# Kernel tuning notes

Measured on AMD Instinct MI355X. Metric: run time of the kernel, lower is better.

The kernel has to match this reference:

```python
import jax, jax.numpy as jnp
import numpy as np

H = 4       # N_head
C = 32      # c_hidden
CZ = 128    # c_z
N = 256
B = 1
EPS = 1e-5


def setup_inputs() -> dict:
    key = jax.random.key(0)
    ks = jax.random.split(key, 8)
    hc = H * C
    return {
        "z": jax.random.normal(ks[0], (B, N, N, CZ), dtype=jnp.float32),
        "ln_scale": jnp.ones((CZ,), dtype=jnp.float32),
        "ln_bias": jnp.zeros((CZ,), dtype=jnp.float32),
        "Wq": jax.random.normal(ks[1], (CZ, hc), dtype=jnp.float32) * 0.02,
        "Wk": jax.random.normal(ks[2], (CZ, hc), dtype=jnp.float32) * 0.02,
        "Wv": jax.random.normal(ks[3], (CZ, hc), dtype=jnp.float32) * 0.02,
        "Wb": jax.random.normal(ks[4], (CZ, H), dtype=jnp.float32) * 0.02,
        "Wg": jax.random.normal(ks[5], (CZ, hc), dtype=jnp.float32) * 0.02,
        "Wo": jax.random.normal(ks[6], (hc, CZ), dtype=jnp.float32) * 0.02,
    }


def reference(z, ln_scale, ln_bias, Wq, Wk, Wv, Wb, Wg, Wo):
    b, n = z.shape[0], z.shape[1]
    # LayerNorm over c_z
    mu = jnp.mean(z, axis=-1, keepdims=True)
    var = jnp.mean(jnp.square(z - mu), axis=-1, keepdims=True)
    zn = (z - mu) * jax.lax.rsqrt(var + EPS) * ln_scale + ln_bias
    # projections -> [B, N, N, H, C]
    q = (zn @ Wq).reshape(b, n, n, H, C)
    k = (zn @ Wk).reshape(b, n, n, H, C)
    v = (zn @ Wv).reshape(b, n, n, H, C)
    bias = zn @ Wb                                  # [B, N, N, H]
    g = jax.nn.sigmoid(zn @ Wg).reshape(b, n, n, H, C)
    # attention around starting node i: query at (i,j), keys/values at (i,k)
    scores = jnp.einsum('bijhd,bikhd->bijkh', q, k) * (1.0 / C ** 0.5)
    scores = scores + bias[:, None, :, :, :]        # bias[b, j, k, h]
    a = jax.nn.softmax(scores, axis=-2)             # softmax over k
    o = jnp.einsum('bijkh,bikhd->bijhd', a, v)      # [B, N, N, H, C]
    o = (g * o).reshape(b, n, n, H * C)
    return o @ Wo
```

## Files before the change

kernel.cpp:

```cpp
#include <hip/hip_runtime.h>
#include <math.h>

#define NN 256
#define CZ 128
#define NH 4
#define CH 32
#define HC 128
#define NPIX (NN*NN)
#define L2E   1.4426950408889634f
#define SCALE2 (0.17677669529663687f * 1.4426950408889634f)

typedef __attribute__((ext_vector_type(8))) short bf16x8;
typedef __attribute__((ext_vector_type(4))) float fx4;
typedef __attribute__((ext_vector_type(4))) unsigned u32x4;

__device__ __forceinline__ unsigned pack_hl(float x) {
    unsigned b  = __builtin_bit_cast(unsigned, x);
    unsigned hb = b & 0xFFFF0000u;
    float r = x - __builtin_bit_cast(float, hb);
    return hb | (__builtin_bit_cast(unsigned, r) >> 16);
}
__device__ __forceinline__ void load_split8(const float* p, bf16x8& h, bf16x8& l) {
    float4 x0 = *(const float4*)p;
    float4 x1 = *(const float4*)(p + 4);
    float xs[8] = {x0.x, x0.y, x0.z, x0.w, x1.x, x1.y, x1.z, x1.w};
    #pragma unroll
    for (int j = 0; j < 8; ++j) {
        unsigned b  = __builtin_bit_cast(unsigned, xs[j]);
        unsigned hb = b & 0xFFFF0000u;
        float r = xs[j] - __builtin_bit_cast(float, hb);
        h[j] = (short)(hb >> 16);
        l[j] = (short)(__builtin_bit_cast(unsigned, r) >> 16);
    }
}
__device__ __forceinline__ void deint_raw(u32x4 e0, u32x4 e1, bf16x8& h, bf16x8& l) {
    unsigned es[8] = {e0[0], e0[1], e0[2], e0[3], e1[0], e1[1], e1[2], e1[3]};
    unsigned hw[4], lw[4];
    #pragma unroll
    for (int j = 0; j < 4; ++j) {
        unsigned a = es[2 * j], b = es[2 * j + 1];
        hw[j] = (a >> 16) | (b & 0xFFFF0000u);
        lw[j] = (a & 0x0000FFFFu) | (b << 16);
    }
    h = __builtin_bit_cast(bf16x8, u32x4{hw[0], hw[1], hw[2], hw[3]});
    l = __builtin_bit_cast(bf16x8, u32x4{lw[0], lw[1], lw[2], lw[3]});
}
__device__ __forceinline__ void deint8(const unsigned* p, bf16x8& h, bf16x8& l) {
    u32x4 e0 = *(const u32x4*)p;
    u32x4 e1 = *(const u32x4*)(p + 4);
    deint_raw(e0, e1, h, l);
}

__device__ __forceinline__ void qtrans(unsigned &x, unsigned &y) {
#if __has_builtin(__builtin_amdgcn_permlane32_swap) && __has_builtin(__builtin_amdgcn_permlane16_swap)
    {
        auto r = __builtin_amdgcn_permlane32_swap(x, y, false, false);
        x = r[0]; y = r[1];
    }
    {
        auto r = __builtin_amdgcn_permlane16_swap(x, y, false, false);
        x = r[0]; y = r[1];
    }
#else
    asm("v_permlane32_swap_b32 %0, %1\n\t"
        "v_permlane16_swap_b32 %0, %1" : "+v"(x), "+v"(y));
#endif
}

__global__ __launch_bounds__(256) void pack_w_kernel(
    const float* __restrict__ Wq, const float* __restrict__ Wk,
    const float* __restrict__ Wv, const float* __restrict__ Wg,
    const float* __restrict__ Wo, bf16x8* __restrict__ pk)
{
    int id  = blockIdx.x * 256 + threadIdx.x;
    int mid = id >> 11;
    int e   = id & 2047;
    const float* W = (mid == 0) ? Wq : (mid == 1) ? Wk : (mid == 2) ? Wv : (mid == 3) ? Wg : Wo;
    int quad = e & 3, n = (e >> 2) & 127, ks = e >> 9;
    int k0 = ks * 32 + quad * 8;
    bf16x8 h, l;
    #pragma unroll
    for (int j = 0; j < 8; ++j) {
        float x = W[(size_t)(k0 + j) * 128 + n];
        unsigned b  = __builtin_bit_cast(unsigned, x);
        unsigned hb = b & 0xFFFF0000u;
        float r = x - __builtin_bit_cast(float, hb);
        h[j] = (short)(hb >> 16);
        l[j] = (short)(__builtin_bit_cast(unsigned, r) >> 16);
    }
    pk[(size_t)mid * 4096 + e]        = h;
    pk[(size_t)mid * 4096 + 2048 + e] = l;
}

__global__ __launch_bounds__(256) void ln_proj_kernel(
    const float* __restrict__ z, const float* __restrict__ ls, const float* __restrict__ lb,
    const float* __restrict__ Wb, const bf16x8* __restrict__ pk,
    unsigned* __restrict__ q_pk, unsigned* __restrict__ k_pk, unsigned* __restrict__ v_pk,
    float* __restrict__ g_ws, float* __restrict__ bias_n)
{
    __shared__ float zsh[32][132];
    __shared__ float rsum[256], rsq[256];
    __shared__ float pmu[32], prs[32];

    const int t  = threadIdx.x;
    const int p0 = blockIdx.x * 32;
    const int i  = p0 >> 8;
    const int j0 = p0 & 255;

    const float4* z4 = (const float4*)(z + (size_t)p0 * CZ);
    #pragma unroll
    for (int r = 0; r < 4; ++r) {
        int idx4 = t + 256 * r;
        int p = idx4 >> 5, pos = idx4 & 31;
        *(float4*)&zsh[p][pos * 4] = z4[idx4];
    }
    __syncthreads();

    {
        int p = t >> 3, sg = t & 7;
        float s = 0.f, q = 0.f;
        #pragma unroll
        for (int u = 0; u < 16; ++u) { float x = zsh[p][sg * 16 + u]; s += x; q += x * x; }
        rsum[t] = s; rsq[t] = q;
    }
    __syncthreads();
    if (t < 32) {
        float s = 0.f, q = 0.f;
        #pragma unroll
        for (int g = 0; g < 8; ++g) { s += rsum[t * 8 + g]; q += rsq[t * 8 + g]; }
        float mu  = s * (1.0f / 128.0f);
        float var = q * (1.0f / 128.0f) - mu * mu;
        float a   = var + 1e-5f;
        float r   = rsqrtf(a);
        r = r * (1.5f - 0.5f * a * r * r);
        pmu[t] = mu; prs[t] = r;
    }
    __syncthreads();

    #pragma unroll
    for (int r4 = 0; r4 < 4; ++r4) {
        int idx4 = t + 256 * r4;
        int p = idx4 >> 5, pos = idx4 & 31;
        float4 v  = *(float4*)&zsh[p][pos * 4];
        float4 s4 = ((const float4*)ls)[pos];
        float4 b4 = ((const float4*)lb)[pos];
        float mu = pmu[p], rs = prs[p];
        v.x = (v.x - mu) * rs * s4.x + b4.x;
        v.y = (v.y - mu) * rs * s4.y + b4.y;
        v.z = (v.z - mu) * rs * s4.z + b4.z;
        v.w = (v.w - mu) * rs * s4.w + b4.w;
        *(float4*)&zsh[p][pos * 4] = v;
    }
    __syncthreads();

    const int wv = t >> 6, lane = t & 63;
    const int lrow = lane & 15, quad = lane >> 4;
    const bf16x8* ph = pk + (size_t)wv * 4096;
    const bf16x8* pl = ph + 2048;

    fx4 acc[2][8];
    #pragma unroll
    for (int mr = 0; mr < 2; ++mr)
        #pragma unroll
        for (int nc = 0; nc < 8; ++nc)
            acc[mr][nc] = fx4{0.f, 0.f, 0.f, 0.f};

    #pragma unroll
    for (int ks = 0; ks < 4; ++ks) {
        bf16x8 ah[2], al[2];
        #pragma unroll
        for (int mr = 0; mr < 2; ++mr)
            load_split8(&zsh[mr * 16 + lrow][ks * 32 + quad * 8], ah[mr], al[mr]);
        #pragma unroll
        for (int nc = 0; nc < 8; ++nc) {
            int bi = (ks * 128 + nc * 16 + lrow) * 4 + quad;
            bf16x8 bh = ph[bi], bl = pl[bi];
            #pragma unroll
            for (int mr = 0; mr < 2; ++mr) {
                acc[mr][nc] = __builtin_amdgcn_mfma_f32_16x16x32_bf16(ah[mr], bl, acc[mr][nc], 0, 0, 0);
                acc[mr][nc] = __builtin_amdgcn_mfma_f32_16x16x32_bf16(al[mr], bh, acc[mr][nc], 0, 0, 0);
                acc[mr][nc] = __builtin_amdgcn_mfma_f32_16x16x32_bf16(ah[mr], bh, acc[mr][nc], 0, 0, 0);
            }
        }
    }

    #pragma unroll
    for (int mr = 0; mr < 2; ++mr) {
        #pragma unroll
        for (int nc = 0; nc < 8; ++nc) {
            int cg = nc * 16 + lrow;
            int h = cg >> 5, cc = cg & 31;
            int jl = mr * 16 + quad * 4;
            fx4 a = acc[mr][nc];
            if (wv == 0) {
                unsigned* qp = q_pk + ((size_t)(i * NH + h) * NN + j0 + jl) * CH + cc;
                #pragma unroll
                for (int r = 0; r < 4; ++r) qp[r * CH] = pack_hl(a[r]);
            } else if (wv == 1) {
                unsigned* kp = k_pk + ((size_t)(i * NH + h) * NN + j0 + jl) * CH + cc;
                #pragma unroll
                for (int r = 0; r < 4; ++r) kp[r * CH] = pack_hl(a[r]);
            } else if (wv == 2) {
                u32x4 e = {pack_hl(a[0]), pack_hl(a[1]), pack_hl(a[2]), pack_hl(a[3])};
                *(u32x4*)(v_pk + ((size_t)(i * NH + h) * CH + cc) * NN + j0 + jl) = e;
            } else {
                float* gp = g_ws + (size_t)(p0 + jl) * HC + cg;
                #pragma unroll
                for (int r = 0; r < 4; ++r) gp[r * HC] = 1.0f / (1.0f + __expf(-a[r]));
            }
        }
    }

    if (t < 128) {
        int hh = t >> 5, p = t & 31;
        float b = 0.f;
        for (int d = 0; d < 128; ++d) b = fmaf(zsh[p][d], Wb[d * 4 + hh], b);
        bias_n[(size_t)hh * NPIX + (size_t)i * NN + j0 + p] = b * L2E;
    }
}

__global__ __launch_bounds__(256) void attn_kernel(
    const unsigned* __restrict__ q_pk, const unsigned* __restrict__ k_pk,
    const unsigned* __restrict__ v_pk, const float* __restrict__ g_ws,
    const float* __restrict__ bias_n, float* __restrict__ go_ws)
{
    const int t = threadIdx.x;
    const int wv = t >> 6, lane = t & 63;
    const int lrow = lane & 15, quad = lane >> 4;
    const int h = blockIdx.x & 3, i = blockIdx.x >> 2;
    const int qb = wv * 64;

    const unsigned* qs = q_pk + (size_t)(i * NH + h) * NN * CH;
    const unsigned* ks = k_pk + (size_t)(i * NH + h) * NN * CH;
    const unsigned* vs = v_pk + (size_t)(i * NH + h) * CH * NN;
    const float*    bs = bias_n + (size_t)h * NPIX;

    bf16x8 qh[4], ql[4];
    #pragma unroll
    for (int nt = 0; nt < 4; ++nt)
        deint8(qs + (size_t)(qb + nt * 16 + lrow) * CH + quad * 8, qh[nt], ql[nt]);

    u32x4 krA[2], krB[2];
    #pragma unroll
    for (int mt = 0; mt < 2; ++mt) {
        const u32x4* kp = (const u32x4*)(ks + (size_t)(mt * 16 + lrow) * CH + quad * 8);
        krA[mt] = kp[0]; krB[mt] = kp[1];
    }

    fx4 oacc[2][4];
    #pragma unroll
    for (int ct = 0; ct < 2; ++ct)
        #pragma unroll
        for (int nt = 0; nt < 4; ++nt)
            oacc[ct][nt] = fx4{0.f, 0.f, 0.f, 0.f};
    float lsum[4] = {0.f, 0.f, 0.f, 0.f};

    for (int kb = 0; kb < NN; kb += 32) {
        u32x4 vrA[2], vrB[2];
        #pragma unroll
        for (int ct = 0; ct < 2; ++ct) {
            const u32x4* vp = (const u32x4*)(vs + (size_t)(ct * 16 + lrow) * NN + kb + quad * 8);
            vrA[ct] = vp[0]; vrB[ct] = vp[1];
        }
        float4 bv[4][2];
        #pragma unroll
        for (int nt = 0; nt < 4; ++nt)
            #pragma unroll
            for (int mt = 0; mt < 2; ++mt)
                bv[nt][mt] = *(const float4*)(bs + (size_t)(qb + nt * 16 + lrow) * NN
                                                 + kb + mt * 16 + quad * 4);
        const int kb2 = (kb + 32) & (NN - 1);
        u32x4 nkA[2], nkB[2];
        #pragma unroll
        for (int mt = 0; mt < 2; ++mt) {
            const u32x4* kp = (const u32x4*)(ks + (size_t)(kb2 + mt * 16 + lrow) * CH + quad * 8);
            nkA[mt] = kp[0]; nkB[mt] = kp[1];
        }

        bf16x8 kh[2], kl_[2];
        #pragma unroll
        for (int mt = 0; mt < 2; ++mt)
            deint_raw(krA[mt], krB[mt], kh[mt], kl_[mt]);

        fx4 sv[4][2];
        __builtin_amdgcn_s_setprio(1);
        #pragma unroll
        for (int nt = 0; nt < 4; ++nt) {
            #pragma unroll
            for (int mt = 0; mt < 2; ++mt) {
                fx4 s = fx4{0.f, 0.f, 0.f, 0.f};
                s = __builtin_amdgcn_mfma_f32_16x16x32_bf16(kh[mt],  ql[nt], s, 0, 0, 0);
                s = __builtin_amdgcn_mfma_f32_16x16x32_bf16(kl_[mt], qh[nt], s, 0, 0, 0);
                s = __builtin_amdgcn_mfma_f32_16x16x32_bf16(kh[mt],  qh[nt], s, 0, 0, 0);
                sv[nt][mt] = s;
            }
        }
        __builtin_amdgcn_s_setprio(0);

        bf16x8 vh[2], vl[2];
        #pragma unroll
        for (int ct = 0; ct < 2; ++ct)
            deint_raw(vrA[ct], vrB[ct], vh[ct], vl[ct]);

        unsigned w0h[4][2], w1h[4][2], w0l[4][2], w1l[4][2];
        #pragma unroll
        for (int nt = 0; nt < 4; ++nt) {
            #pragma unroll
            for (int mt = 0; mt < 2; ++mt) {
                fx4 s = sv[nt][mt];
                float4 b4 = bv[nt][mt];
                float e0 = exp2f(fmaf(s[0], SCALE2, b4.x));
                float e1 = exp2f(fmaf(s[1], SCALE2, b4.y));
                float e2 = exp2f(fmaf(s[2], SCALE2, b4.z));
                float e3 = exp2f(fmaf(s[3], SCALE2, b4.w));
                lsum[nt] += (e0 + e1) + (e2 + e3);

                unsigned b0 = __builtin_bit_cast(unsigned, e0);
                unsigned b1 = __builtin_bit_cast(unsigned, e1);
                unsigned b2 = __builtin_bit_cast(unsigned, e2);
                unsigned b3 = __builtin_bit_cast(unsigned, e3);
                unsigned h01 = (b0 >> 16) | (b1 & 0xFFFF0000u);
                unsigned h23 = (b2 >> 16) | (b3 & 0xFFFF0000u);
                float r0 = e0 - __builtin_bit_cast(float, b0 & 0xFFFF0000u);
                float r1 = e1 - __builtin_bit_cast(float, b1 & 0xFFFF0000u);
                float r2 = e2 - __builtin_bit_cast(float, b2 & 0xFFFF0000u);
                float r3 = e3 - __builtin_bit_cast(float, b3 & 0xFFFF0000u);
                unsigned l01 = (__builtin_bit_cast(unsigned, r0) >> 16)
                             | (__builtin_bit_cast(unsigned, r1) & 0xFFFF0000u);
                unsigned l23 = (__builtin_bit_cast(unsigned, r2) >> 16)
                             | (__builtin_bit_cast(unsigned, r3) & 0xFFFF0000u);
                w0h[nt][mt] = h01; w1h[nt][mt] = h23;
                w0l[nt][mt] = l01; w1l[nt][mt] = l23;
            }
        }

        #pragma unroll
        for (int nt = 0; nt < 4; ++nt) {
            qtrans(w0h[nt][0], w0h[nt][1]);
            qtrans(w1h[nt][0], w1h[nt][1]);
            qtrans(w0l[nt][0], w0l[nt][1]);
            qtrans(w1l[nt][0], w1l[nt][1]);
        }

        __builtin_amdgcn_s_setprio(1);
        #pragma unroll
        for (int nt = 0; nt < 4; ++nt) {
            bf16x8 pbh = __builtin_bit_cast(bf16x8,
                u32x4{w0h[nt][0], w1h[nt][0], w0h[nt][1], w1h[nt][1]});
            bf16x8 pbl = __builtin_bit_cast(bf16x8,
                u32x4{w0l[nt][0], w1l[nt][0], w0l[nt][1], w1l[nt][1]});
            #pragma unroll
            for (int ct = 0; ct < 2; ++ct) {
                oacc[ct][nt] = __builtin_amdgcn_mfma_f32_16x16x32_bf16(vh[ct], pbl, oacc[ct][nt], 0, 0, 0);
                oacc[ct][nt] = __builtin_amdgcn_mfma_f32_16x16x32_bf16(vl[ct], pbh, oacc[ct][nt], 0, 0, 0);
                oacc[ct][nt] = __builtin_amdgcn_mfma_f32_16x16x32_bf16(vh[ct], pbh, oacc[ct][nt], 0, 0, 0);
            }
        }
        __builtin_amdgcn_s_setprio(0);

        #pragma unroll
        for (int mt = 0; mt < 2; ++mt) { krA[mt] = nkA[mt]; krB[mt] = nkB[mt]; }
    }

    #pragma unroll
    for (int nt = 0; nt < 4; ++nt) {
        float s = lsum[nt];
        s += __shfl_xor(s, 16, 64);
        s += __shfl_xor(s, 32, 64);
        float inv = 1.0f / s;
        size_t pix = (size_t)i * NN + qb + nt * 16 + lrow;
        #pragma unroll
        for (int ct = 0; ct < 2; ++ct) {
            const float* gp = g_ws + pix * HC + h * CH + ct * 16 + quad * 4;
            float4 g4 = *(const float4*)gp;
            fx4 o = oacc[ct][nt];
            float4 r;
            r.x = g4.x * o[0] * inv;
            r.y = g4.y * o[1] * inv;
            r.z = g4.z * o[2] * inv;
            r.w = g4.w * o[3] * inv;
            *(float4*)(go_ws + pix * HC + h * CH + ct * 16 + quad * 4) = r;
        }
    }
}

__global__ __launch_bounds__(256) void outproj_kernel(
    const float* __restrict__ go_ws, const bf16x8* __restrict__ pk, float* __restrict__ out)
{
    __shared__ float gsh[64][132];
    const int t  = threadIdx.x;
    const int p0 = blockIdx.x * 64;

    const float4* g4 = (const float4*)(go_ws + (size_t)p0 * HC);
    #pragma unroll
    for (int r = 0; r < 8; ++r) {
        int idx4 = t + 256 * r;
        int p = idx4 >> 5, pos = idx4 & 31;
        *(float4*)&gsh[p][pos * 4] = g4[idx4];
    }
    __syncthreads();

    const int wv = t >> 6, lane = t & 63;
    const int lrow = lane & 15, quad = lane >> 4;
    const bf16x8* ph = pk + (size_t)4 * 4096;
    const bf16x8* pl = ph + 2048;

    fx4 acc[8];
    #pragma unroll
    for (int nc = 0; nc < 8; ++nc) acc[nc] = fx4{0.f, 0.f, 0.f, 0.f};

    #pragma unroll
    for (int ks = 0; ks < 4; ++ks) {
        bf16x8 ah, al;
        load_split8(&gsh[wv * 16 + lrow][ks * 32 + quad * 8], ah, al);
        #pragma unroll
        for (int nc = 0; nc < 8; ++nc) {
            int bi = (ks * 128 + nc * 16 + lrow) * 4 + quad;
            bf16x8 bh = ph[bi], bl = pl[bi];
            acc[nc] = __builtin_amdgcn_mfma_f32_16x16x32_bf16(ah, bl, acc[nc], 0, 0, 0);
            acc[nc] = __builtin_amdgcn_mfma_f32_16x16x32_bf16(al, bh, acc[nc], 0, 0, 0);
            acc[nc] = __builtin_amdgcn_mfma_f32_16x16x32_bf16(ah, bh, acc[nc], 0, 0, 0);
        }
    }

    #pragma unroll
    for (int nc = 0; nc < 8; ++nc) {
        #pragma unroll
        for (int r = 0; r < 4; ++r)
            out[(size_t)(p0 + wv * 16 + quad * 4 + r) * HC + nc * 16 + lrow] = acc[nc][r];
    }
}

extern "C" void kernel_launch(void* const* d_in, const int* in_sizes, int n_in,
                              void* d_out, int out_size, void* d_ws, size_t ws_size,
                              hipStream_t stream)
{
    const float* z  = (const float*)d_in[0];
    const float* ls = (const float*)d_in[1];
    const float* lb = (const float*)d_in[2];
    const float* Wq = (const float*)d_in[3];
    const float* Wk = (const float*)d_in[4];
    const float* Wv = (const float*)d_in[5];
    const float* Wb = (const float*)d_in[6];
    const float* Wg = (const float*)d_in[7];
    const float* Wo = (const float*)d_in[8];

    float* ws = (float*)d_ws;
    const size_t BIG = (size_t)NPIX * HC;
    unsigned* q_pk  = (unsigned*)ws;
    unsigned* k_pk  = (unsigned*)(ws + BIG);
    unsigned* v_pk  = (unsigned*)(ws + 2 * BIG);
    float* g_ws     = ws + 3 * BIG;
    float* go_ws    = ws + 4 * BIG;
    float* bias_n   = ws + 5 * BIG;
    bf16x8* pk      = (bf16x8*)(bias_n + (size_t)NH * NPIX);

    pack_w_kernel<<<40, 256, 0, stream>>>(Wq, Wk, Wv, Wg, Wo, pk);
    ln_proj_kernel<<<NPIX / 32, 256, 0, stream>>>(z, ls, lb, Wb, pk,
                                                  q_pk, k_pk, v_pk, g_ws, bias_n);
    attn_kernel<<<NN * NH, 256, 0, stream>>>(q_pk, k_pk, v_pk, g_ws, bias_n, go_ws);
    outproj_kernel<<<NPIX / 64, 256, 0, stream>>>(go_ws, pk, (float*)d_out);
}
```

Measured before the change: 246.5 us.

## Use register LayerNorm with shuffles, stage Wb in LDS, and skip LDS in outproj

The LayerNorm step now loads each pixel's row directly into registers and reduces the sum and sum of squares with warp shuffles. This replaces the LDS partial-sum arrays and two of the block barriers. The bias projection now reads Wb from shared memory and uses all 256 threads, with pairs of threads splitting the reduction dimension. The output projection loads the gated activations straight from global memory into registers instead of staging them through LDS, which removes a barrier but makes the global reads less coalesced.

Measured after the change: 246.2 us. Within noise of the previous version (-0.2%).

```diff
diff --git a/kernel.cpp b/kernel.cpp
--- a/kernel.cpp
+++ b/kernel.cpp
@@ -99,57 +99,52 @@
     float* __restrict__ g_ws, float* __restrict__ bias_n)
 {
     __shared__ float zsh[32][132];
-    __shared__ float rsum[256], rsq[256];
-    __shared__ float pmu[32], prs[32];
+    __shared__ float wbsh[512];
 
     const int t  = threadIdx.x;
     const int p0 = blockIdx.x * 32;
     const int i  = p0 >> 8;
     const int j0 = p0 & 255;
 
-    const float4* z4 = (const float4*)(z + (size_t)p0 * CZ);
+    wbsh[t]       = Wb[t];
+    wbsh[t + 256] = Wb[t + 256];
+
+    const int p = t >> 3, sub = t & 7;
+    float4 zv[4];
+    {
+        const float4* zp = (const float4*)(z + (size_t)(p0 + p) * CZ + sub * 16);
+        #pragma unroll
+        for (int r = 0; r < 4; ++r) zv[r] = zp[r];
+    }
+    float s = 0.f, q = 0.f;
     #pragma unroll
     for (int r = 0; r < 4; ++r) {
-        int idx4 = t + 256 * r;
-        int p = idx4 >> 5, pos = idx4 & 31;
-        *(float4*)&zsh[p][pos * 4] = z4[idx4];
-    }
-    __syncthreads();
-
+        s += ((zv[r].x + zv[r].y) + (zv[r].z + zv[r].w));
+        q += ((zv[r].x * zv[r].x + zv[r].y * zv[r].y)
+            + (zv[r].z * zv[r].z + zv[r].w * zv[r].w));
+    }
+    #pragma unroll
+    for (int m = 1; m <= 4; m <<= 1) {
+        s += __shfl_xor(s, m, 64);
+        q += __shfl_xor(q, m, 64);
+    }
     {
-        int p = t >> 3, sg = t & 7;
-        float s = 0.f, q = 0.f;
-        #pragma unroll
-        for (int u = 0; u < 16; ++u) { float x = zsh[p][sg * 16 + u]; s += x; q += x * x; }
-        rsum[t] = s; rsq[t] = q;
-    }
-    __syncthreads();
-    if (t < 32) {
-        float s = 0.f, q = 0.f;
-        #pragma unroll
-        for (int g = 0; g < 8; ++g) { s += rsum[t * 8 + g]; q += rsq[t * 8 + g]; }
         float mu  = s * (1.0f / 128.0f);
         float var = q * (1.0f / 128.0f) - mu * mu;
         float a   = var + 1e-5f;
-        float r   = rsqrtf(a);
-        r = r * (1.5f - 0.5f * a * r * r);
-        pmu[t] = mu; prs[t] = r;
-    }
-    __syncthreads();
-
-    #pragma unroll
-    for (int r4 = 0; r4 < 4; ++r4) {
-        int idx4 = t + 256 * r4;
-        int p = idx4 >> 5, pos = idx4 & 31;
-        float4 v  = *(float4*)&zsh[p][pos * 4];
-        float4 s4 = ((const float4*)ls)[pos];
-        float4 b4 = ((const float4*)lb)[pos];
-        float mu = pmu[p], rs = prs[p];
-        v.x = (v.x - mu) * rs * s4.x + b4.x;
-        v.y = (v.y - mu) * rs * s4.y + b4.y;
-        v.z = (v.z - mu) * rs * s4.z + b4.z;
-        v.w = (v.w - mu) * rs * s4.w + b4.w;
-        *(float4*)&zsh[p][pos * 4] = v;
+        float r0  = rsqrtf(a);
+        r0 = r0 * (1.5f - 0.5f * a * r0 * r0);
+        #pragma unroll
+        for (int r = 0; r < 4; ++r) {
+            float4 s4 = ((const float4*)ls)[sub * 4 + r];
+            float4 b4 = ((const float4*)lb)[sub * 4 + r];
+            float4 v  = zv[r];
+            v.x = (v.x - mu) * r0 * s4.x + b4.x;
+            v.y = (v.y - mu) * r0 * s4.y + b4.y;
+            v.z = (v.z - mu) * r0 * s4.z + b4.z;
+            v.w = (v.w - mu) * r0 * s4.w + b4.w;
+            *(float4*)&zsh[p][sub * 16 + r * 4] = v;
+        }
     }
     __syncthreads();
 
@@ -211,11 +206,17 @@
         }
     }
 
-    if (t < 128) {
-        int hh = t >> 5, p = t & 31;
+    {
+        int pair = t >> 1, half = t & 1;
+        int hh = pair >> 5, pp = pair & 31;
+        int d0 = half * 64;
         float b = 0.f;
-        for (int d = 0; d < 128; ++d) b = fmaf(zsh[p][d], Wb[d * 4 + hh], b);
-        bias_n[(size_t)hh * NPIX + (size_t)i * NN + j0 + p] = b * L2E;
+        #pragma unroll 8
+        for (int d = 0; d < 64; ++d)
+            b = fmaf(zsh[pp][d0 + d], wbsh[(d0 + d) * 4 + hh], b);
+        b += __shfl_xor(b, 1, 64);
+        if (half == 0)
+            bias_n[(size_t)hh * NPIX + (size_t)i * NN + j0 + pp] = b * L2E;
     }
 }
 
@@ -387,39 +388,33 @@
 __global__ __launch_bounds__(256) void outproj_kernel(
     const float* __restrict__ go_ws, const bf16x8* __restrict__ pk, float* __restrict__ out)
 {
-    __shared__ float gsh[64][132];
     const int t  = threadIdx.x;
     const int p0 = blockIdx.x * 64;
-
-    const float4* g4 = (const float4*)(go_ws + (size_t)p0 * HC);
-    #pragma unroll
-    for (int r = 0; r < 8; ++r) {
-        int idx4 = t + 256 * r;
-        int p = idx4 >> 5, pos = idx4 & 31;
-        *(float4*)&gsh[p][pos * 4] = g4[idx4];
-    }
-    __syncthreads();
-
     const int wv = t >> 6, lane = t & 63;
     const int lrow = lane & 15, quad = lane >> 4;
     const bf16x8* ph = pk + (size_t)4 * 4096;
     const bf16x8* pl = ph + 2048;
 
+    const float* grow = go_ws + (size_t)(p0 + wv * 16 + lrow) * HC + quad * 8;
+
+    bf16x8 ah[4], al[4];
+    #pragma unroll
+    for (int ks = 0; ks < 4; ++ks)
+        load_split8(grow + ks * 32, ah[ks], al[ks]);
+
     fx4 acc[8];
     #pragma unroll
     for (int nc = 0; nc < 8; ++nc) acc[nc] = fx4{0.f, 0.f, 0.f, 0.f};
 
     #pragma unroll
     for (int ks = 0; ks < 4; ++ks) {
-        bf16x8 ah, al;
-        load_split8(&gsh[wv * 16 + lrow][ks * 32 + quad * 8], ah, al);
         #pragma unroll
         for (int nc = 0; nc < 8; ++nc) {
             int bi = (ks * 128 + nc * 16 + lrow) * 4 + quad;
             bf16x8 bh = ph[bi], bl = pl[bi];
-            acc[nc] = __builtin_amdgcn_mfma_f32_16x16x32_bf16(ah, bl, acc[nc], 0, 0, 0);
-            acc[nc] = __builtin_amdgcn_mfma_f32_16x16x32_bf16(al, bh, acc[nc], 0, 0, 0);
-            acc[nc] = __builtin_amdgcn_mfma_f32_16x16x32_bf16(ah, bh, acc[nc], 0, 0, 0);
+            acc[nc] = __builtin_amdgcn_mfma_f32_16x16x32_bf16(ah[ks], bl, acc[nc], 0, 0, 0);
+            acc[nc] = __builtin_amdgcn_mfma_f32_16x16x32_bf16(al[ks], bh, acc[nc], 0, 0, 0);
+            acc[nc] = __builtin_amdgcn_mfma_f32_16x16x32_bf16(ah[ks], bh, acc[nc], 0, 0, 0);
         }
     }
 
```
